# Kernel tuning notes

Hardware: AMD Instinct MI355X
Metric: run time of the kernel (lower is better)

## Reference

```python
import jax, jax.numpy as jnp
import numpy as np

B, S, D, U = 32, 2048, 1024, 1024


def setup_inputs() -> dict:
    key = jax.random.key(0)
    ks = jax.random.split(key, 10)
    s = 0.02
    return {
        "dec_hidden": jax.random.normal(ks[0], (B, D), jnp.float32),
        "enc_output": jax.random.normal(ks[1], (B, S, D), jnp.float32),
        "enc_pad_mask": jnp.ones((B, S), jnp.int32),  # accepted but unused, as in the original
        "use_coverage": True,
        "prev_coverage": jax.random.uniform(ks[2], (B, S, 1), jnp.float32),
        "Ws_w": jax.random.normal(ks[3], (D, U), jnp.float32) * s,
        "Ws_b": jnp.zeros((U,), jnp.float32),
        "Wh_w": jax.random.normal(ks[4], (D, U), jnp.float32) * s,
        "Wh_b": jnp.zeros((U,), jnp.float32),
        "Wc_w": jax.random.normal(ks[5], (1, U), jnp.float32) * s,
        "Wc_b": jnp.zeros((U,), jnp.float32),
        "V_w": jax.random.normal(ks[6], (U, 1), jnp.float32) * s,
        "V_b": jnp.zeros((1,), jnp.float32),
    }


def reference(dec_hidden, enc_output, enc_pad_mask, use_coverage, prev_coverage,
              Ws_w, Ws_b, Wh_w, Wh_b, Wc_w, Wc_b, V_w, V_b):
    # W_h(dec_hidden) with time axis: [B, 1, U]
    h = (dec_hidden @ Wh_w + Wh_b)[:, None, :]
    # W_s(enc_output): [B, S, U]
    feat = jnp.einsum('bsd,du->bsu', enc_output, Ws_w) + Ws_b + h
    if use_coverage and prev_coverage is not None:
        # W_c(prev_coverage): [B, S, 1] @ [1, U] -> [B, S, U]
        feat = feat + prev_coverage @ Wc_w + Wc_b
        score = jnp.tanh(feat) @ V_w + V_b            # [B, S, 1]
        attention_weights = jax.nn.softmax(score, axis=1)
        coverage = attention_weights + prev_coverage
    else:
        score = jnp.tanh(feat) @ V_w + V_b
        attention_weights = jax.nn.softmax(score, axis=1)
        coverage = attention_weights if use_coverage else []
    # weighted sum over sequence axis: [B, D]
    context_vector = jnp.sum(attention_weights * enc_output, axis=1)
    return context_vector, jnp.squeeze(attention_weights, -1), coverage
```

## Files before the change

kernel.cpp:

```cpp
#include <hip/hip_runtime.h>
#include <hip/hip_bf16.h>

namespace {

constexpr int kB = 32;
constexpr int kS = 2048;
constexpr int kD = 1024;
constexpr int kU = 1024;

constexpr int BM = 256;
constexpr int BN = 256;
constexpr int BK = 64;
constexpr int kKT = kD / BK;
constexpr int kMT = (kB * kS) / BM;
constexpr int kNT = kU / BN;
constexpr size_t kHalf = 16384;
constexpr size_t kTileChunk = 2 * kHalf;
constexpr size_t kPanel = (size_t)kKT * kTileChunk;

typedef __attribute__((ext_vector_type(8))) short bf16x8;
typedef __attribute__((ext_vector_type(4))) float f32x4;

__device__ __forceinline__ unsigned short f2bf(float x) {
  union { __hip_bfloat16 h; unsigned short u; } c;
  c.h = __float2bfloat16(x);
  return c.u;
}

__device__ __forceinline__ float bf2f(unsigned short u) {
  union { unsigned int i; float f; } c;
  c.i = ((unsigned int)u) << 16;
  return c.f;
}

__device__ __forceinline__ float tanh_fast(float x) {
  float e = __expf(2.0f * x);
  return 1.0f - 2.0f * __builtin_amdgcn_rcpf(e + 1.0f);
}

__device__ __forceinline__ void gload16(const void* g, void* l) {
  __builtin_amdgcn_global_load_lds(
      (const __attribute__((address_space(1))) void*)g,
      (__attribute__((address_space(3))) void*)l, 16, 0, 0);
}


__global__ __launch_bounds__(256) void h2_kernel(
    const float* __restrict__ dec, const float* __restrict__ Whw,
    const float* __restrict__ Whb, const float* __restrict__ Wsb,
    const float* __restrict__ Wcb, float* __restrict__ h2) {
  const int b = blockIdx.y;
  const int u = blockIdx.x * 256 + threadIdx.x;
  float acc = Whb[u] + Wsb[u] + Wcb[u];
  const float* dh = dec + b * kD;
  #pragma unroll 8
  for (int d = 0; d < kD; ++d) acc += dh[d] * Whw[(size_t)d * kU + u];
  h2[b * kU + u] = acc;
}


__global__ __launch_bounds__(256) void convA_kernel(
    const float* __restrict__ enc, unsigned char* __restrict__ encT) {
  const size_t e = ((size_t)blockIdx.x * 256 + threadIdx.x) * 8;
  const int r = (int)(e >> 10), d0 = (int)(e & 1023);
  float4 v0 = *(const float4*)(enc + e);
  float4 v1 = *(const float4*)(enc + e + 4);
  uint4 p;
  p.x = (unsigned)f2bf(v0.x) | ((unsigned)f2bf(v0.y) << 16);
  p.y = (unsigned)f2bf(v0.z) | ((unsigned)f2bf(v0.w) << 16);
  p.z = (unsigned)f2bf(v1.x) | ((unsigned)f2bf(v1.y) << 16);
  p.w = (unsigned)f2bf(v1.z) | ((unsigned)f2bf(v1.w) << 16);
  const int mt = r >> 8, rh = (r >> 7) & 1, row = r & 127;
  const int kt = d0 >> 6, c8 = (d0 & 63) >> 3;
  unsigned char* dst = encT + (size_t)mt * kPanel + (size_t)kt * kTileChunk +
                       (size_t)rh * kHalf + row * 128 +
                       (((unsigned)c8 << 4) ^ (((unsigned)row & 7) << 4));
  *(uint4*)dst = p;
}

__global__ __launch_bounds__(256) void tpose2_kernel(
    const float* __restrict__ W, unsigned char* __restrict__ Bt) {
  __shared__ float tile[32][33];
  const int u0 = blockIdx.x * 32, d0 = blockIdx.y * 32;
  const int tx = threadIdx.x, ty = threadIdx.y;
  #pragma unroll
  for (int i = 0; i < 4; ++i)
    tile[ty + i * 8][tx] = W[(size_t)(d0 + ty + i * 8) * kU + u0 + tx];
  __syncthreads();
  #pragma unroll
  for (int i = 0; i < 4; ++i) {
    const int u = u0 + ty + i * 8, d = d0 + tx;
    const int nt = u >> 8, gh = (u >> 7) & 1, n = u & 127;
    const int kt = d >> 6, c = d & 63;
    *(unsigned short*)(Bt + (size_t)nt * kPanel + (size_t)kt * kTileChunk +
                       (size_t)gh * kHalf + n * 128 +
                       (((((unsigned)c >> 3) << 4) ^ (((unsigned)n & 7) << 4)) +
                        (c & 7) * 2)) = f2bf(tile[tx][ty + i * 8]);
  }
}

#define MFMA_BF16(a, b, c) __builtin_amdgcn_mfma_f32_16x16x32_bf16((a), (b), (c), 0, 0, 0)

__global__ __launch_bounds__(512, 2) void score_gemm3_kernel(
    const unsigned char* __restrict__ encT, const unsigned char* __restrict__ Bt,
    const float* __restrict__ h2, const float* __restrict__ pc,
    const float* __restrict__ Wcw, const float* __restrict__ Vw,
    float* __restrict__ scorep) {
  __shared__ __attribute__((aligned(16))) unsigned char lds[131072];

  const int tid = threadIdx.x;
  const int lane = tid & 63;
  const int w = tid >> 6;
  const int lr = lane & 15, lq = lane >> 4;
  const int wrow = (w >> 2) * 64;
  const int wcs = w & 3;
  const int bg = wcs >> 1;
  const int wncol = (wcs & 1) * 64;

  const int work = (blockIdx.x & 7) * 128 + (blockIdx.x >> 3);
  const int mtile = work >> 2, ntile = work & 3;

  const unsigned char* Ab = encT + (size_t)mtile * kPanel;
  const unsigned char* Bb = Bt + (size_t)ntile * kPanel;
  const int so0 = tid * 16;
  const int so1 = tid * 16 + 8192;

  f32x4 acc[2][4][4];
  #pragma unroll
  for (int h = 0; h < 2; ++h)
    #pragma unroll
    for (int i = 0; i < 4; ++i)
      #pragma unroll
      for (int j = 0; j < 4; ++j) acc[h][i][j] = (f32x4){0.f, 0.f, 0.f, 0.f};

  {
    const unsigned char* At = Ab;
    const unsigned char* Btt = Bb;
    gload16(At + so0, lds + 0 + so0);
    gload16(At + so1, lds + 0 + so1);
    gload16(Btt + so0, lds + 65536 + so0);
    gload16(Btt + so1, lds + 65536 + so1);
    gload16(Btt + kHalf + so0, lds + 65536 + kHalf + so0);
    gload16(Btt + kHalf + so1, lds + 65536 + kHalf + so1);
    gload16(At + kHalf + so0, lds + kHalf + so0);
    gload16(At + kHalf + so1, lds + kHalf + so1);
  }

  for (int t = 0; t < kKT - 1; ++t) {
    const int p = t & 1;
    const int aP = p * 2 * (int)kHalf;
    const int aQ = (1 - p) * 2 * (int)kHalf;
    const int bP = 65536 + p * 2 * (int)kHalf;
    const int bQ = 65536 + (1 - p) * 2 * (int)kHalf;
    const unsigned char* An = Ab + (size_t)(t + 1) * kTileChunk;
    const unsigned char* Bn = Bb + (size_t)(t + 1) * kTileChunk;

    gload16(An + so0, lds + aQ + so0);
    gload16(An + so1, lds + aQ + so1);
    gload16(Bn + so0, lds + bQ + so0);
    gload16(Bn + so1, lds + bQ + so1);
    gload16(Bn + (int)kHalf + so0, lds + bQ + (int)kHalf + so0);
    gload16(Bn + (int)kHalf + so1, lds + bQ + (int)kHalf + so1);
    asm volatile("s_waitcnt vmcnt(8)" ::: "memory");
    __builtin_amdgcn_s_barrier();
    __builtin_amdgcn_sched_barrier(0);

    bf16x8 bfr[4][2];
    #pragma unroll
    for (int cf = 0; cf < 4; ++cf)
      #pragma unroll
      for (int ks = 0; ks < 2; ++ks) {
        const int n = wncol + cf * 16 + lr;
        bfr[cf][ks] = *(const bf16x8*)(lds + bP + bg * (int)kHalf + n * 128 +
                                       ((ks * 64 + lq * 16) ^ ((n & 7) << 4)));
      }
    #pragma unroll
    for (int ks = 0; ks < 2; ++ks) {
      bf16x8 af[4];
      #pragma unroll
      for (int rf = 0; rf < 4; ++rf) {
        const int row = wrow + rf * 16 + lr;
        af[rf] = *(const bf16x8*)(lds + aP + row * 128 +
                                  ((ks * 64 + lq * 16) ^ ((row & 7) << 4)));
      }
      __builtin_amdgcn_s_setprio(1);
      #pragma unroll
      for (int rf = 0; rf < 4; ++rf)
        #pragma unroll
        for (int cf = 0; cf < 4; ++cf)
          acc[0][rf][cf] = MFMA_BF16(af[rf], bfr[cf][ks], acc[0][rf][cf]);
      __builtin_amdgcn_s_setprio(0);
    }

    gload16(An + (int)kHalf + so0, lds + aQ + (int)kHalf + so0);
    gload16(An + (int)kHalf + so1, lds + aQ + (int)kHalf + so1);
    asm volatile("s_waitcnt vmcnt(8)" ::: "memory");
    __builtin_amdgcn_s_barrier();
    __builtin_amdgcn_sched_barrier(0);

    #pragma unroll
    for (int ks = 0; ks < 2; ++ks) {
      bf16x8 af[4];
      #pragma unroll
      for (int rf = 0; rf < 4; ++rf) {
        const int row = wrow + rf * 16 + lr;
        af[rf] = *(const bf16x8*)(lds + aP + (int)kHalf + row * 128 +
                                  ((ks * 64 + lq * 16) ^ ((row & 7) << 4)));
      }
      __builtin_amdgcn_s_setprio(1);
      #pragma unroll
      for (int rf = 0; rf < 4; ++rf)
        #pragma unroll
        for (int cf = 0; cf < 4; ++cf)
          acc[1][rf][cf] = MFMA_BF16(af[rf], bfr[cf][ks], acc[1][rf][cf]);
      __builtin_amdgcn_s_setprio(0);
    }
  }

  {
    const int p = (kKT - 1) & 1;
    const int aP = p * 2 * (int)kHalf;
    const int bP = 65536 + p * 2 * (int)kHalf;

    asm volatile("s_waitcnt vmcnt(2)" ::: "memory");
    __builtin_amdgcn_s_barrier();
    __builtin_amdgcn_sched_barrier(0);

    bf16x8 bfr[4][2];
    #pragma unroll
    for (int cf = 0; cf < 4; ++cf)
      #pragma unroll
      for (int ks = 0; ks < 2; ++ks) {
        const int n = wncol + cf * 16 + lr;
        bfr[cf][ks] = *(const bf16x8*)(lds + bP + bg * (int)kHalf + n * 128 +
                                       ((ks * 64 + lq * 16) ^ ((n & 7) << 4)));
      }
    #pragma unroll
    for (int ks = 0; ks < 2; ++ks) {
      bf16x8 af[4];
      #pragma unroll
      for (int rf = 0; rf < 4; ++rf) {
        const int row = wrow + rf * 16 + lr;
        af[rf] = *(const bf16x8*)(lds + aP + row * 128 +
                                  ((ks * 64 + lq * 16) ^ ((row & 7) << 4)));
      }
      #pragma unroll
      for (int rf = 0; rf < 4; ++rf)
        #pragma unroll
        for (int cf = 0; cf < 4; ++cf)
          acc[0][rf][cf] = MFMA_BF16(af[rf], bfr[cf][ks], acc[0][rf][cf]);
    }

    asm volatile("s_waitcnt vmcnt(0)" ::: "memory");
    __builtin_amdgcn_s_barrier();
    __builtin_amdgcn_sched_barrier(0);

    #pragma unroll
    for (int ks = 0; ks < 2; ++ks) {
      bf16x8 af[4];
      #pragma unroll
      for (int rf = 0; rf < 4; ++rf) {
        const int row = wrow + rf * 16 + lr;
        af[rf] = *(const bf16x8*)(lds + aP + (int)kHalf + row * 128 +
                                  ((ks * 64 + lq * 16) ^ ((row & 7) << 4)));
      }
      #pragma unroll
      for (int rf = 0; rf < 4; ++rf)
        #pragma unroll
        for (int cf = 0; cf < 4; ++cf)
          acc[1][rf][cf] = MFMA_BF16(af[rf], bfr[cf][ks], acc[1][rf][cf]);
    }
  }

  const int bidx = mtile >> 3;
  float hv[4], wv[4], vv[4];
  #pragma unroll
  for (int cf = 0; cf < 4; ++cf) {
    const int u = ntile * BN + wcs * 64 + cf * 16 + lr;
    hv[cf] = h2[bidx * kU + u];
    wv[cf] = Wcw[u];
    vv[cf] = Vw[u];
  }
  float* plane = scorep + (size_t)(ntile * 4 + wcs) * (kB * kS);
  #pragma unroll
  for (int h = 0; h < 2; ++h) {
    #pragma unroll
    for (int rf = 0; rf < 4; ++rf) {
      #pragma unroll
      for (int j = 0; j < 4; ++j) {
        const int r = mtile * BM + h * 128 + wrow + rf * 16 + lq * 4 + j;
        const float pcv = pc[r];
        float partial = 0.f;
        #pragma unroll
        for (int cf = 0; cf < 4; ++cf) {
          const float feat = acc[h][rf][cf][j] + hv[cf] + pcv * wv[cf];
          partial += tanh_fast(feat) * vv[cf];
        }
        partial += __shfl_xor(partial, 1);
        partial += __shfl_xor(partial, 2);
        partial += __shfl_xor(partial, 4);
        partial += __shfl_xor(partial, 8);
        if (lr == 0) plane[r] = partial;
      }
    }
  }
}

__global__ __launch_bounds__(256) void softmax2_kernel(
    const float* __restrict__ scorep, const float* __restrict__ pc,
    float* __restrict__ attn, float* __restrict__ cov) {
  const int b = blockIdx.x, tid = threadIdx.x;
  const int lane = tid & 63, wid = tid >> 6;
  const size_t base = (size_t)b * kS + tid * 8;
  float v[8] = {0.f, 0.f, 0.f, 0.f, 0.f, 0.f, 0.f, 0.f};
  #pragma unroll
  for (int p = 0; p < 16; ++p) {
    const float* s = scorep + (size_t)p * (kB * kS) + base;
    float4 a = *(const float4*)(s);
    float4 c = *(const float4*)(s + 4);
    v[0] += a.x; v[1] += a.y; v[2] += a.z; v[3] += a.w;
    v[4] += c.x; v[5] += c.y; v[6] += c.z; v[7] += c.w;
  }
  float m = v[0];
  #pragma unroll
  for (int i = 1; i < 8; ++i) m = fmaxf(m, v[i]);
  #pragma unroll
  for (int msk = 1; msk < 64; msk <<= 1) m = fmaxf(m, __shfl_xor(m, msk));
  __shared__ float redm[4], reds[4];
  if (lane == 0) redm[wid] = m;
  __syncthreads();
  m = fmaxf(fmaxf(redm[0], redm[1]), fmaxf(redm[2], redm[3]));
  float e[8], sum = 0.f;
  #pragma unroll
  for (int i = 0; i < 8; ++i) { e[i] = __expf(v[i] - m); sum += e[i]; }
  #pragma unroll
  for (int msk = 1; msk < 64; msk <<= 1) sum += __shfl_xor(sum, msk);
  if (lane == 0) reds[wid] = sum;
  __syncthreads();
  sum = reds[0] + reds[1] + reds[2] + reds[3];
  const float inv = 1.0f / sum;
  float pv[8], a[8], c[8];
  const float* p = pc + base;
  *(float4*)(pv) = *(const float4*)(p);
  *(float4*)(pv + 4) = *(const float4*)(p + 4);
  #pragma unroll
  for (int i = 0; i < 8; ++i) { a[i] = e[i] * inv; c[i] = a[i] + pv[i]; }
  *(float4*)(attn + base) = *(float4*)(a);
  *(float4*)(attn + base + 4) = *(float4*)(a + 4);
  *(float4*)(cov + base) = *(float4*)(c);
  *(float4*)(cov + base + 4) = *(float4*)(c + 4);
}

__global__ __launch_bounds__(256) void context2_kernel(
    const unsigned char* __restrict__ encT, const float* __restrict__ attn,
    float* __restrict__ ctx) {
  const int kt = blockIdx.x;
  const int b = blockIdx.y;
  const int cg = threadIdx.x & 7;
  const int rgrp = threadIdx.x >> 3;
  float acc8[8];
  #pragma unroll
  for (int j = 0; j < 8; ++j) acc8[j] = 0.f;
  const float* ab = attn + (size_t)b * kS;
  for (int it = 0; it < kS / 32; ++it) {
    const int s = it * 32 + rgrp;
    const int r = b * kS + s;
    const int mt = r >> 8, rh = (r >> 7) & 1, row = r & 127;
    const unsigned char* chunk = encT + (size_t)mt * kPanel +
                                 (size_t)kt * kTileChunk + (size_t)rh * kHalf;
    uint4 v = *(const uint4*)(chunk + row * 128 +
                              ((((unsigned)cg << 4) ^ (((unsigned)row & 7) << 4))));
    const float a = ab[s];
    const unsigned int* vw = (const unsigned int*)&v;
    #pragma unroll
    for (int q = 0; q < 4; ++q) {
      acc8[2 * q]     += a * bf2f((unsigned short)(vw[q] & 0xffff));
      acc8[2 * q + 1] += a * bf2f((unsigned short)(vw[q] >> 16));
    }
  }
  __shared__ float red[256 * 8];
  #pragma unroll
  for (int j = 0; j < 8; ++j) red[threadIdx.x * 8 + j] = acc8[j];
  __syncthreads();
  if (rgrp < 8) {
  }
  for (int stride = 16; stride > 0; stride >>= 1) {
    if (rgrp < stride) {
      #pragma unroll
      for (int j = 0; j < 8; ++j)
        red[(rgrp * 8 + cg) * 8 + j] += red[((rgrp + stride) * 8 + cg) * 8 + j];
    }
    __syncthreads();
  }
  if (rgrp == 0) {
    #pragma unroll
    for (int j = 0; j < 8; ++j)
      ctx[(size_t)b * kD + kt * 64 + cg * 8 + j] = red[cg * 8 + j];
  }
}


__global__ __launch_bounds__(256) void tpose_fb_kernel(
    const float* __restrict__ W, unsigned short* __restrict__ out) {
  __shared__ float tile[32][33];
  const int u0 = blockIdx.x * 32, d0 = blockIdx.y * 32;
  const int tx = threadIdx.x, ty = threadIdx.y;
  #pragma unroll
  for (int i = 0; i < 4; ++i)
    tile[ty + i * 8][tx] = W[(size_t)(d0 + ty + i * 8) * kU + u0 + tx];
  __syncthreads();
  #pragma unroll
  for (int i = 0; i < 4; ++i)
    out[(size_t)(u0 + ty + i * 8) * kD + d0 + tx] = f2bf(tile[tx][ty + i * 8]);
}

__global__ __launch_bounds__(256, 2) void score_gemm_fb_kernel(
    const float* __restrict__ enc, const unsigned short* __restrict__ WsT,
    const float* __restrict__ h2, const float* __restrict__ pc,
    const float* __restrict__ Wcw, const float* __restrict__ Vw,
    float* __restrict__ score) {
  __shared__ __attribute__((aligned(16))) unsigned char smA[128 * 64 * 2];
  __shared__ __attribute__((aligned(16))) unsigned char smB[128 * 64 * 2];
  const int tid = threadIdx.x;
  const int lane = tid & 63;
  const int wid = tid >> 6;
  const int wr = wid >> 1, wc = wid & 1;
  const int mtile = blockIdx.x >> 3, ntile = blockIdx.x & 7;
  const int r0 = mtile * 128, n0 = ntile * 128;
  f32x4 acc[4][4];
  #pragma unroll
  for (int i = 0; i < 4; ++i)
    #pragma unroll
    for (int j = 0; j < 4; ++j) acc[i][j] = (f32x4){0.f, 0.f, 0.f, 0.f};
  const int kqA = tid & 15;
  const int rowA = tid >> 4;
  const int kcB = tid & 7;
  const int nB = tid >> 3;
  float4 aReg[8];
  uint4 bReg[4];
  #pragma unroll
  for (int i = 0; i < 8; ++i)
    aReg[i] = *(const float4*)(enc + (size_t)(r0 + rowA + 16 * i) * kD + kqA * 4);
  #pragma unroll
  for (int i = 0; i < 4; ++i)
    bReg[i] = *(const uint4*)(WsT + (size_t)(n0 + nB + 32 * i) * kD + kcB * 8);
  const int lr = lane & 15, lq = lane >> 4;
  for (int k0 = 0; k0 < kD; k0 += 64) {
    #pragma unroll
    for (int i = 0; i < 8; ++i) {
      const int row = rowA + 16 * i;
      uint2 p;
      p.x = (unsigned)f2bf(aReg[i].x) | ((unsigned)f2bf(aReg[i].y) << 16);
      p.y = (unsigned)f2bf(aReg[i].z) | ((unsigned)f2bf(aReg[i].w) << 16);
      *(uint2*)(smA + row * 128 + ((kqA * 8) ^ ((row & 7) << 4))) = p;
    }
    #pragma unroll
    for (int i = 0; i < 4; ++i) {
      const int n = nB + 32 * i;
      *(uint4*)(smB + n * 128 + ((kcB * 16) ^ ((n & 7) << 4))) = bReg[i];
    }
    __syncthreads();
    if (k0 + 64 < kD) {
      const int kn = k0 + 64;
      #pragma unroll
      for (int i = 0; i < 8; ++i)
        aReg[i] = *(const float4*)(enc + (size_t)(r0 + rowA + 16 * i) * kD + kn + kqA * 4);
      #pragma unroll
      for (int i = 0; i < 4; ++i)
        bReg[i] = *(const uint4*)(WsT + (size_t)(n0 + nB + 32 * i) * kD + kn + kcB * 8);
    }
    #pragma unroll
    for (int ks = 0; ks < 2; ++ks) {
      const int kb = ks * 64 + lq * 16;
      bf16x8 af[4], bfr[4];
      #pragma unroll
      for (int fm = 0; fm < 4; ++fm) {
        const int row = wr * 64 + fm * 16 + lr;
        af[fm] = *(const bf16x8*)(smA + row * 128 + (kb ^ ((row & 7) << 4)));
      }
      #pragma unroll
      for (int fn = 0; fn < 4; ++fn) {
        const int n = wc * 64 + fn * 16 + lr;
        bfr[fn] = *(const bf16x8*)(smB + n * 128 + (kb ^ ((n & 7) << 4)));
      }
      #pragma unroll
      for (int fm = 0; fm < 4; ++fm)
        #pragma unroll
        for (int fn = 0; fn < 4; ++fn)
          acc[fm][fn] = MFMA_BF16(af[fm], bfr[fn], acc[fm][fn]);
    }
    __syncthreads();
  }
  const int bidx = r0 >> 11;
  float hv[4], wv[4], vv[4];
  #pragma unroll
  for (int fn = 0; fn < 4; ++fn) {
    const int u = n0 + wc * 64 + fn * 16 + lr;
    hv[fn] = h2[bidx * kU + u];
    wv[fn] = Wcw[u];
    vv[fn] = Vw[u];
  }
  #pragma unroll
  for (int fm = 0; fm < 4; ++fm) {
    #pragma unroll
    for (int j = 0; j < 4; ++j) {
      const int r = r0 + wr * 64 + fm * 16 + lq * 4 + j;
      const float pcv = pc[r];
      float partial = 0.f;
      #pragma unroll
      for (int fn = 0; fn < 4; ++fn) {
        const float feat = acc[fm][fn][j] + hv[fn] + pcv * wv[fn];
        partial += tanh_fast(feat) * vv[fn];
      }
      partial += __shfl_xor(partial, 1);
      partial += __shfl_xor(partial, 2);
      partial += __shfl_xor(partial, 4);
      partial += __shfl_xor(partial, 8);
      if (lr == 0) atomicAdd(&score[r], partial);
    }
  }
}

__global__ __launch_bounds__(256) void softmax_fb_kernel(
    const float* __restrict__ score, const float* __restrict__ pc,
    float* __restrict__ attn, float* __restrict__ cov) {
  const int b = blockIdx.x, tid = threadIdx.x;
  const int lane = tid & 63, wid = tid >> 6;
  const float* s = score + (size_t)b * kS;
  float v[8];
  *(float4*)(v) = *(const float4*)(s + tid * 8);
  *(float4*)(v + 4) = *(const float4*)(s + tid * 8 + 4);
  float m = v[0];
  #pragma unroll
  for (int i = 1; i < 8; ++i) m = fmaxf(m, v[i]);
  #pragma unroll
  for (int msk = 1; msk < 64; msk <<= 1) m = fmaxf(m, __shfl_xor(m, msk));
  __shared__ float redm[4], reds[4];
  if (lane == 0) redm[wid] = m;
  __syncthreads();
  m = fmaxf(fmaxf(redm[0], redm[1]), fmaxf(redm[2], redm[3]));
  float e[8], sum = 0.f;
  #pragma unroll
  for (int i = 0; i < 8; ++i) { e[i] = __expf(v[i] - m); sum += e[i]; }
  #pragma unroll
  for (int msk = 1; msk < 64; msk <<= 1) sum += __shfl_xor(sum, msk);
  if (lane == 0) reds[wid] = sum;
  __syncthreads();
  sum = reds[0] + reds[1] + reds[2] + reds[3];
  const float inv = 1.0f / sum;
  float pv[8], a[8], c[8];
  const float* p = pc + (size_t)b * kS + tid * 8;
  *(float4*)(pv) = *(const float4*)(p);
  *(float4*)(pv + 4) = *(const float4*)(p + 4);
  #pragma unroll
  for (int i = 0; i < 8; ++i) { a[i] = e[i] * inv; c[i] = a[i] + pv[i]; }
  *(float4*)(attn + (size_t)b * kS + tid * 8) = *(float4*)(a);
  *(float4*)(attn + (size_t)b * kS + tid * 8 + 4) = *(float4*)(a + 4);
  *(float4*)(cov + (size_t)b * kS + tid * 8) = *(float4*)(c);
  *(float4*)(cov + (size_t)b * kS + tid * 8 + 4) = *(float4*)(c + 4);
}

__global__ __launch_bounds__(256) void context_fb_kernel(
    const float* __restrict__ enc, const float* __restrict__ attn,
    float* __restrict__ ctx) {
  const int b = blockIdx.z;
  const int s0 = blockIdx.y * 256;
  const int d = blockIdx.x * 256 + threadIdx.x;
  const float* e = enc + ((size_t)b * kS + s0) * kD + d;
  const float* a = attn + (size_t)b * kS + s0;
  float acc = 0.f;
  #pragma unroll 8
  for (int s = 0; s < 256; ++s) acc += a[s] * e[(size_t)s * kD];
  atomicAdd(&ctx[b * kD + d], acc);
}

}

extern "C" void kernel_launch(void* const* d_in, const int* in_sizes, int n_in,
                              void* d_out, int out_size, void* d_ws, size_t ws_size,
                              hipStream_t stream) {
  (void)in_sizes; (void)n_in; (void)out_size;
  const float* dec = (const float*)d_in[0];
  const float* enc = (const float*)d_in[1];
  const float* pc  = (const float*)d_in[4];
  const float* Wsw = (const float*)d_in[5];
  const float* Wsb = (const float*)d_in[6];
  const float* Whw = (const float*)d_in[7];
  const float* Whb = (const float*)d_in[8];
  const float* Wcw = (const float*)d_in[9];
  const float* Wcb = (const float*)d_in[10];
  const float* Vw  = (const float*)d_in[11];

  float* ctx  = (float*)d_out;
  float* attn = (float*)d_out + kB * kD;
  float* cov  = attn + kB * kS;

  unsigned char* ws = (unsigned char*)d_ws;

  const size_t encT_sz = (size_t)kB * kS * kD * 2;
  const size_t Bt_sz   = (size_t)kU * kD * 2;
  const size_t h2_sz   = (size_t)kB * kU * 4;
  const size_t sp_sz   = (size_t)16 * kB * kS * 4;
  const size_t need    = encT_sz + Bt_sz + h2_sz + sp_sz;

  if (ws_size >= need) {
    unsigned char* encT = ws;
    unsigned char* Bt   = ws + encT_sz;
    float* h2     = (float*)(ws + encT_sz + Bt_sz);
    float* scorep = (float*)(ws + encT_sz + Bt_sz + h2_sz);

    convA_kernel<<<dim3((kB * kS * kD / 8) / 256), 256, 0, stream>>>(enc, encT);
    tpose2_kernel<<<dim3(kU / 32, kD / 32), dim3(32, 8), 0, stream>>>(Wsw, Bt);
    h2_kernel<<<dim3(kU / 256, kB), 256, 0, stream>>>(dec, Whw, Whb, Wsb, Wcb, h2);
    score_gemm3_kernel<<<dim3(kMT * kNT), 512, 0, stream>>>(
        encT, Bt, h2, pc, Wcw, Vw, scorep);
    softmax2_kernel<<<dim3(kB), 256, 0, stream>>>(scorep, pc, attn, cov);
    context2_kernel<<<dim3(kD / 64, kB), 256, 0, stream>>>(encT, attn, ctx);
  } else {
    unsigned short* WsT = (unsigned short*)ws;
    float* h2    = (float*)(ws + (size_t)2 * 1024 * 1024);
    float* score = (float*)(ws + (size_t)2 * 1024 * 1024 + 131072);
    hipMemsetAsync(score, 0, kB * kS * sizeof(float), stream);
    hipMemsetAsync(ctx, 0, kB * kD * sizeof(float), stream);
    h2_kernel<<<dim3(kU / 256, kB), 256, 0, stream>>>(dec, Whw, Whb, Wsb, Wcb, h2);
    tpose_fb_kernel<<<dim3(kU / 32, kD / 32), dim3(32, 8), 0, stream>>>(Wsw, WsT);
    score_gemm_fb_kernel<<<dim3(4096), 256, 0, stream>>>(
        enc, WsT, h2, pc, Wcw, Vw, score);
    softmax_fb_kernel<<<dim3(kB), 256, 0, stream>>>(score, pc, attn, cov);
    context_fb_kernel<<<dim3(kD / 256, kS / 256, kB), 256, 0, stream>>>(enc, attn, ctx);
  }
}
```

Baseline: 310.6 us.

## Restructure score GEMM into 8-phase ping-pong schedule with per-wave 128-row tiles

```diff
diff --git a/kernel.cpp b/kernel.cpp
--- a/kernel.cpp
+++ b/kernel.cpp
@@ -45,17 +45,17 @@
 }
 
 
-__global__ __launch_bounds__(256) void h2_kernel(
+__global__ __launch_bounds__(256) void h2b_kernel(
     const float* __restrict__ dec, const float* __restrict__ Whw,
     const float* __restrict__ Whb, const float* __restrict__ Wsb,
     const float* __restrict__ Wcb, float* __restrict__ h2) {
-  const int b = blockIdx.y;
-  const int u = blockIdx.x * 256 + threadIdx.x;
-  float acc = Whb[u] + Wsb[u] + Wcb[u];
+  const int u = blockIdx.x * 64 + (threadIdx.x & 63);
+  const int b = blockIdx.y * 4 + (threadIdx.x >> 6);
+  float acc = 0.f;
   const float* dh = dec + b * kD;
   #pragma unroll 8
   for (int d = 0; d < kD; ++d) acc += dh[d] * Whw[(size_t)d * kU + u];
-  h2[b * kU + u] = acc;
+  h2[b * kU + u] = acc + Whb[u] + Wsb[u] + Wcb[u];
 }
 
 
@@ -101,7 +101,56 @@
 
 #define MFMA_BF16(a, b, c) __builtin_amdgcn_mfma_f32_16x16x32_bf16((a), (b), (c), 0, 0, 0)
 
-__global__ __launch_bounds__(512, 2) void score_gemm3_kernel(
+#define READ_A8(AF, ABASE, QR)                                                 \
+  _Pragma("unroll")                                                            \
+  for (int rfl = 0; rfl < 4; ++rfl) {                                          \
+    _Pragma("unroll")                                                          \
+    for (int ks = 0; ks < 2; ++ks) {                                           \
+      const int row_ = ((QR)*4 + rfl) * 16 + lr;                               \
+      AF[rfl][ks] = *(const bf16x8*)((ABASE) + row_ * 128 +                    \
+                                     ((ks * 64 + lq * 16) ^ ((lr & 7) << 4))); \
+    }                                                                          \
+  }
+
+#define READ_B4(BF, BBASE, QC)                                                 \
+  _Pragma("unroll")                                                            \
+  for (int cfl = 0; cfl < 2; ++cfl) {                                          \
+    _Pragma("unroll")                                                          \
+    for (int ks = 0; ks < 2; ++ks) {                                           \
+      const int row_ = ((QC)*2 + cfl) * 16 + lr;                               \
+      BF[cfl][ks] = *(const bf16x8*)((BBASE) + row_ * 128 +                    \
+                                     ((ks * 64 + lq * 16) ^ ((lr & 7) << 4))); \
+    }                                                                          \
+  }
+
+#define MF16(QR, QC, AF, BF)                                                   \
+  _Pragma("unroll")                                                            \
+  for (int ks = 0; ks < 2; ++ks) {                                             \
+    _Pragma("unroll")                                                          \
+    for (int rfl = 0; rfl < 4; ++rfl) {                                        \
+      _Pragma("unroll")                                                        \
+      for (int cfl = 0; cfl < 2; ++cfl)                                        \
+        acc[(QR)*4 + rfl][(QC)*2 + cfl] =                                      \
+            MFMA_BF16(AF[rfl][ks], BF[cfl][ks], acc[(QR)*4 + rfl][(QC)*2 + cfl]); \
+    }                                                                          \
+  }
+
+#define STAGE2(GSRC, LDST)                                                     \
+  gload16((GSRC) + so0, (LDST) + so0);                                         \
+  gload16((GSRC) + so1, (LDST) + so1);
+
+#define BAR_IN                                                                 \
+  __builtin_amdgcn_s_barrier();                                                \
+  asm volatile("s_waitcnt lgkmcnt(0)" ::: "memory");                           \
+  __builtin_amdgcn_sched_barrier(0);                                           \
+  __builtin_amdgcn_s_setprio(1);
+
+#define BAR_OUT                                                                \
+  __builtin_amdgcn_s_setprio(0);                                               \
+  __builtin_amdgcn_sched_barrier(0);                                           \
+  __builtin_amdgcn_s_barrier();
+
+__global__ __launch_bounds__(512, 1) void score_gemm4_kernel(
     const unsigned char* __restrict__ encT, const unsigned char* __restrict__ Bt,
     const float* __restrict__ h2, const float* __restrict__ pc,
     const float* __restrict__ Wcw, const float* __restrict__ Vw,
@@ -112,10 +161,9 @@
   const int lane = tid & 63;
   const int w = tid >> 6;
   const int lr = lane & 15, lq = lane >> 4;
-  const int wrow = (w >> 2) * 64;
-  const int wcs = w & 3;
-  const int bg = wcs >> 1;
-  const int wncol = (wcs & 1) * 64;
+  const int wm = w >> 2;
+  const int wn = w & 3;
+  const int g = wn >> 1;
 
   const int work = (blockIdx.x & 7) * 128 + (blockIdx.x >> 3);
   const int mtile = work >> 2, ntile = work & 3;
@@ -125,183 +173,105 @@
   const int so0 = tid * 16;
   const int so1 = tid * 16 + 8192;
 
-  f32x4 acc[2][4][4];
-  #pragma unroll
-  for (int h = 0; h < 2; ++h)
-    #pragma unroll
-    for (int i = 0; i < 4; ++i)
-      #pragma unroll
-      for (int j = 0; j < 4; ++j) acc[h][i][j] = (f32x4){0.f, 0.f, 0.f, 0.f};
-
-  {
-    const unsigned char* At = Ab;
-    const unsigned char* Btt = Bb;
-    gload16(At + so0, lds + 0 + so0);
-    gload16(At + so1, lds + 0 + so1);
-    gload16(Btt + so0, lds + 65536 + so0);
-    gload16(Btt + so1, lds + 65536 + so1);
-    gload16(Btt + kHalf + so0, lds + 65536 + kHalf + so0);
-    gload16(Btt + kHalf + so1, lds + 65536 + kHalf + so1);
-    gload16(At + kHalf + so0, lds + kHalf + so0);
-    gload16(At + kHalf + so1, lds + kHalf + so1);
-  }
-
-  for (int t = 0; t < kKT - 1; ++t) {
-    const int p = t & 1;
-    const int aP = p * 2 * (int)kHalf;
-    const int aQ = (1 - p) * 2 * (int)kHalf;
-    const int bP = 65536 + p * 2 * (int)kHalf;
-    const int bQ = 65536 + (1 - p) * 2 * (int)kHalf;
-    const unsigned char* An = Ab + (size_t)(t + 1) * kTileChunk;
-    const unsigned char* Bn = Bb + (size_t)(t + 1) * kTileChunk;
-
-    gload16(An + so0, lds + aQ + so0);
-    gload16(An + so1, lds + aQ + so1);
-    gload16(Bn + so0, lds + bQ + so0);
-    gload16(Bn + so1, lds + bQ + so1);
-    gload16(Bn + (int)kHalf + so0, lds + bQ + (int)kHalf + so0);
-    gload16(Bn + (int)kHalf + so1, lds + bQ + (int)kHalf + so1);
-    asm volatile("s_waitcnt vmcnt(8)" ::: "memory");
-    __builtin_amdgcn_s_barrier();
-    __builtin_amdgcn_sched_barrier(0);
-
-    bf16x8 bfr[4][2];
-    #pragma unroll
-    for (int cf = 0; cf < 4; ++cf)
-      #pragma unroll
-      for (int ks = 0; ks < 2; ++ks) {
-        const int n = wncol + cf * 16 + lr;
-        bfr[cf][ks] = *(const bf16x8*)(lds + bP + bg * (int)kHalf + n * 128 +
-                                       ((ks * 64 + lq * 16) ^ ((n & 7) << 4)));
-      }
-    #pragma unroll
-    for (int ks = 0; ks < 2; ++ks) {
-      bf16x8 af[4];
-      #pragma unroll
-      for (int rf = 0; rf < 4; ++rf) {
-        const int row = wrow + rf * 16 + lr;
-        af[rf] = *(const bf16x8*)(lds + aP + row * 128 +
-                                  ((ks * 64 + lq * 16) ^ ((row & 7) << 4)));
-      }
-      __builtin_amdgcn_s_setprio(1);
-      #pragma unroll
-      for (int rf = 0; rf < 4; ++rf)
-        #pragma unroll
-        for (int cf = 0; cf < 4; ++cf)
-          acc[0][rf][cf] = MFMA_BF16(af[rf], bfr[cf][ks], acc[0][rf][cf]);
-      __builtin_amdgcn_s_setprio(0);
-    }
-
-    gload16(An + (int)kHalf + so0, lds + aQ + (int)kHalf + so0);
-    gload16(An + (int)kHalf + so1, lds + aQ + (int)kHalf + so1);
-    asm volatile("s_waitcnt vmcnt(8)" ::: "memory");
-    __builtin_amdgcn_s_barrier();
-    __builtin_amdgcn_sched_barrier(0);
-
-    #pragma unroll
-    for (int ks = 0; ks < 2; ++ks) {
-      bf16x8 af[4];
-      #pragma unroll
-      for (int rf = 0; rf < 4; ++rf) {
-        const int row = wrow + rf * 16 + lr;
-        af[rf] = *(const bf16x8*)(lds + aP + (int)kHalf + row * 128 +
-                                  ((ks * 64 + lq * 16) ^ ((row & 7) << 4)));
-      }
-      __builtin_amdgcn_s_setprio(1);
-      #pragma unroll
-      for (int rf = 0; rf < 4; ++rf)
-        #pragma unroll
-        for (int cf = 0; cf < 4; ++cf)
-          acc[1][rf][cf] = MFMA_BF16(af[rf], bfr[cf][ks], acc[1][rf][cf]);
-      __builtin_amdgcn_s_setprio(0);
-    }
-  }
-
-  {
-    const int p = (kKT - 1) & 1;
-    const int aP = p * 2 * (int)kHalf;
-    const int bP = 65536 + p * 2 * (int)kHalf;
-
-    asm volatile("s_waitcnt vmcnt(2)" ::: "memory");
-    __builtin_amdgcn_s_barrier();
-    __builtin_amdgcn_sched_barrier(0);
-
-    bf16x8 bfr[4][2];
-    #pragma unroll
-    for (int cf = 0; cf < 4; ++cf)
-      #pragma unroll
-      for (int ks = 0; ks < 2; ++ks) {
-        const int n = wncol + cf * 16 + lr;
-        bfr[cf][ks] = *(const bf16x8*)(lds + bP + bg * (int)kHalf + n * 128 +
-                                       ((ks * 64 + lq * 16) ^ ((n & 7) << 4)));
-      }
-    #pragma unroll
-    for (int ks = 0; ks < 2; ++ks) {
-      bf16x8 af[4];
-      #pragma unroll
-      for (int rf = 0; rf < 4; ++rf) {
-        const int row = wrow + rf * 16 + lr;
-        af[rf] = *(const bf16x8*)(lds + aP + row * 128 +
-                                  ((ks * 64 + lq * 16) ^ ((row & 7) << 4)));
-      }
-      #pragma unroll
-      for (int rf = 0; rf < 4; ++rf)
-        #pragma unroll
-        for (int cf = 0; cf < 4; ++cf)
-          acc[0][rf][cf] = MFMA_BF16(af[rf], bfr[cf][ks], acc[0][rf][cf]);
-    }
-
-    asm volatile("s_waitcnt vmcnt(0)" ::: "memory");
-    __builtin_amdgcn_s_barrier();
-    __builtin_amdgcn_sched_barrier(0);
-
-    #pragma unroll
-    for (int ks = 0; ks < 2; ++ks) {
-      bf16x8 af[4];
-      #pragma unroll
-      for (int rf = 0; rf < 4; ++rf) {
-        const int row = wrow + rf * 16 + lr;
-        af[rf] = *(const bf16x8*)(lds + aP + (int)kHalf + row * 128 +
-                                  ((ks * 64 + lq * 16) ^ ((row & 7) << 4)));
-      }
-      #pragma unroll
-      for (int rf = 0; rf < 4; ++rf)
-        #pragma unroll
-        for (int cf = 0; cf < 4; ++cf)
-          acc[1][rf][cf] = MFMA_BF16(af[rf], bfr[cf][ks], acc[1][rf][cf]);
-    }
-  }
+  unsigned char* Ad0 = lds + (size_t)wm * kHalf;
+  unsigned char* Ad1 = lds + (2 + wm) * kHalf;
+  unsigned char* Bd0 = lds + 65536 + (size_t)g * kHalf + (wn & 1) * 8192;
+  unsigned char* Bd1 = lds + 65536 + (2 + g) * kHalf + (wn & 1) * 8192;
+  unsigned char* aSlot[2][2] = {{lds, lds + kHalf}, {lds + 2 * kHalf, lds + 3 * kHalf}};
+  unsigned char* bSlot[2][2] = {{lds + 65536, lds + 65536 + kHalf},
+                                {lds + 65536 + 2 * kHalf, lds + 65536 + 3 * kHalf}};
+
+  f32x4 acc[8][4];
+  #pragma unroll
+  for (int i = 0; i < 8; ++i)
+    #pragma unroll
+    for (int j = 0; j < 4; ++j) acc[i][j] = (f32x4){0.f, 0.f, 0.f, 0.f};
+
+  bf16x8 af[4][2], b0[2][2], b1[2][2];
+
+  STAGE2(Bb, bSlot[0][0]);
+  STAGE2(Bb + kHalf, bSlot[0][1]);
+  STAGE2(Ab, aSlot[0][0]);
+  STAGE2(Ab + kHalf, aSlot[0][1]);
+  STAGE2(Bb + kTileChunk, bSlot[1][0]);
+  STAGE2(Bb + kTileChunk + kHalf, bSlot[1][1]);
+  asm volatile("s_waitcnt vmcnt(4)" ::: "memory");
+  __builtin_amdgcn_s_barrier();
+  __builtin_amdgcn_sched_barrier(0);
+
+  for (int i = 0; i < kKT / 2; ++i) {
+    const int t2 = (i < kKT / 2 - 1) ? 2 * i + 2 : 2 * i;
+    const int t3 = (i < kKT / 2 - 1) ? 2 * i + 3 : 2 * i;
+    const unsigned char* sA1 = Ab + (size_t)(2 * i + 1) * kTileChunk;
+    const unsigned char* sA2 = Ab + (size_t)t2 * kTileChunk;
+    const unsigned char* sB2 = Bb + (size_t)t2 * kTileChunk;
+    const unsigned char* sB3 = Bb + (size_t)t3 * kTileChunk;
+
+    READ_A8(af, Ad0, 0);
+    READ_B4(b0, Bd0, 0);
+    STAGE2(sA1, aSlot[1][0]);
+    asm volatile("s_waitcnt lgkmcnt(8)" ::: "memory");
+    BAR_IN; MF16(0, 0, af, b0); BAR_OUT;
+
+    READ_B4(b1, Bd0, 1);
+    STAGE2(sA1 + kHalf, aSlot[1][1]);
+    BAR_IN; MF16(0, 1, af, b1); BAR_OUT;
+
+    READ_A8(af, Ad0, 1);
+    STAGE2(sB2, bSlot[0][0]);
+    BAR_IN; MF16(1, 0, af, b0); BAR_OUT;
+
+    STAGE2(sB2 + kHalf, bSlot[0][1]);
+    asm volatile("s_waitcnt vmcnt(4)" ::: "memory");
+    BAR_IN; MF16(1, 1, af, b1); BAR_OUT;
+
+    READ_A8(af, Ad1, 0);
+    READ_B4(b0, Bd1, 0);
+    STAGE2(sA2, aSlot[0][0]);
+    asm volatile("s_waitcnt lgkmcnt(8)" ::: "memory");
+    BAR_IN; MF16(0, 0, af, b0); BAR_OUT;
+
+    READ_B4(b1, Bd1, 1);
+    STAGE2(sA2 + kHalf, aSlot[0][1]);
+    BAR_IN; MF16(0, 1, af, b1); BAR_OUT;
+
+    READ_A8(af, Ad1, 1);
+    STAGE2(sB3, bSlot[1][0]);
+    BAR_IN; MF16(1, 0, af, b0); BAR_OUT;
+
+    STAGE2(sB3 + kHalf, bSlot[1][1]);
+    asm volatile("s_waitcnt vmcnt(4)" ::: "memory");
+    BAR_IN; MF16(1, 1, af, b1); BAR_OUT;
+  }
+  asm volatile("s_waitcnt vmcnt(0)" ::: "memory");
 
   const int bidx = mtile >> 3;
   float hv[4], wv[4], vv[4];
   #pragma unroll
   for (int cf = 0; cf < 4; ++cf) {
-    const int u = ntile * BN + wcs * 64 + cf * 16 + lr;
+    const int u = ntile * BN + wn * 64 + cf * 16 + lr;
     hv[cf] = h2[bidx * kU + u];
     wv[cf] = Wcw[u];
     vv[cf] = Vw[u];
   }
-  float* plane = scorep + (size_t)(ntile * 4 + wcs) * (kB * kS);
-  #pragma unroll
-  for (int h = 0; h < 2; ++h) {
-    #pragma unroll
-    for (int rf = 0; rf < 4; ++rf) {
-      #pragma unroll
-      for (int j = 0; j < 4; ++j) {
-        const int r = mtile * BM + h * 128 + wrow + rf * 16 + lq * 4 + j;
-        const float pcv = pc[r];
-        float partial = 0.f;
-        #pragma unroll
-        for (int cf = 0; cf < 4; ++cf) {
-          const float feat = acc[h][rf][cf][j] + hv[cf] + pcv * wv[cf];
-          partial += tanh_fast(feat) * vv[cf];
-        }
-        partial += __shfl_xor(partial, 1);
-        partial += __shfl_xor(partial, 2);
-        partial += __shfl_xor(partial, 4);
-        partial += __shfl_xor(partial, 8);
-        if (lr == 0) plane[r] = partial;
+  float* plane = scorep + (size_t)(ntile * 4 + wn) * (kB * kS);
+  #pragma unroll
+  for (int rf = 0; rf < 8; ++rf) {
+    #pragma unroll
+    for (int j = 0; j < 4; ++j) {
+      const int r = mtile * BM + wm * 128 + rf * 16 + lq * 4 + j;
+      const float pcv = pc[r];
+      float partial = 0.f;
+      #pragma unroll
+      for (int cf = 0; cf < 4; ++cf) {
+        const float feat = acc[rf][cf][j] + hv[cf] + pcv * wv[cf];
+        partial += tanh_fast(feat) * vv[cf];
       }
+      partial += __shfl_xor(partial, 1);
+      partial += __shfl_xor(partial, 2);
+      partial += __shfl_xor(partial, 4);
+      partial += __shfl_xor(partial, 8);
+      if (lr == 0) plane[r] = partial;
     }
   }
 }
@@ -382,8 +352,6 @@
   #pragma unroll
   for (int j = 0; j < 8; ++j) red[threadIdx.x * 8 + j] = acc8[j];
   __syncthreads();
-  if (rgrp < 8) {
-  }
   for (int stride = 16; stride > 0; stride >>= 1) {
     if (rgrp < stride) {
       #pragma unroll
@@ -472,11 +440,11 @@
     #pragma unroll
     for (int ks = 0; ks < 2; ++ks) {
       const int kb = ks * 64 + lq * 16;
-      bf16x8 af[4], bfr[4];
+      bf16x8 af2[4], bfr[4];
       #pragma unroll
       for (int fm = 0; fm < 4; ++fm) {
         const int row = wr * 64 + fm * 16 + lr;
-        af[fm] = *(const bf16x8*)(smA + row * 128 + (kb ^ ((row & 7) << 4)));
+        af2[fm] = *(const bf16x8*)(smA + row * 128 + (kb ^ ((row & 7) << 4)));
       }
       #pragma unroll
       for (int fn = 0; fn < 4; ++fn) {
@@ -487,7 +455,7 @@
       for (int fm = 0; fm < 4; ++fm)
         #pragma unroll
         for (int fn = 0; fn < 4; ++fn)
-          acc[fm][fn] = MFMA_BF16(af[fm], bfr[fn], acc[fm][fn]);
+          acc[fm][fn] = MFMA_BF16(af2[fm], bfr[fn], acc[fm][fn]);
     }
     __syncthreads();
   }
@@ -611,8 +579,8 @@
 
     convA_kernel<<<dim3((kB * kS * kD / 8) / 256), 256, 0, stream>>>(enc, encT);
     tpose2_kernel<<<dim3(kU / 32, kD / 32), dim3(32, 8), 0, stream>>>(Wsw, Bt);
-    h2_kernel<<<dim3(kU / 256, kB), 256, 0, stream>>>(dec, Whw, Whb, Wsb, Wcb, h2);
-    score_gemm3_kernel<<<dim3(kMT * kNT), 512, 0, stream>>>(
+    h2b_kernel<<<dim3(kU / 64, kB / 4), 256, 0, stream>>>(dec, Whw, Whb, Wsb, Wcb, h2);
+    score_gemm4_kernel<<<dim3(kMT * kNT), 512, 0, stream>>>(
         encT, Bt, h2, pc, Wcw, Vw, scorep);
     softmax2_kernel<<<dim3(kB), 256, 0, stream>>>(scorep, pc, attn, cov);
     context2_kernel<<<dim3(kD / 64, kB), 256, 0, stream>>>(encT, attn, ctx);
@@ -622,7 +590,7 @@
     float* score = (float*)(ws + (size_t)2 * 1024 * 1024 + 131072);
     hipMemsetAsync(score, 0, kB * kS * sizeof(float), stream);
     hipMemsetAsync(ctx, 0, kB * kD * sizeof(float), stream);
-    h2_kernel<<<dim3(kU / 256, kB), 256, 0, stream>>>(dec, Whw, Whb, Wsb, Wcb, h2);
+    h2b_kernel<<<dim3(kU / 64, kB / 4), 256, 0, stream>>>(dec, Whw, Whb, Wsb, Wcb, h2);
     tpose_fb_kernel<<<dim3(kU / 32, kD / 32), dim3(32, 8), 0, stream>>>(Wsw, WsT);
     score_gemm_fb_kernel<<<dim3(4096), 256, 0, stream>>>(
         enc, WsT, h2, pc, Wcw, Vw, score);
```

Result: no change. 315.8 us (+1.6%).
